# Kernel optimization log

Hardware: AMD Instinct MI355X
Metric: run time of the kernel (lower is better)

Reference implementation:

```python
import jax, jax.numpy as jnp
import numpy as np

N = 50000      # nodes
E = 800000     # edges
T = 2000000    # triplets
FE = 64        # num_edge_features
FT = 64        # num_triplet_features
CUTOFF = 6.0   # cutoff_triplet
EPS = 1e-5     # BatchNorm1d eps


def setup_inputs() -> dict:
    key = jax.random.key(0)
    ks = jax.random.split(key, 20)
    rn = lambda k, shape, s=1.0: jax.random.normal(k, shape, dtype=jnp.float32) * s
    inp = {}
    inp["pos"] = rn(ks[0], (N, 3), 3.0)
    inp["nbr_shift"] = rn(ks[1], (E, 3), 0.1)
    inp["edge_attr"] = rn(ks[2], (E, FE))
    inp["triplet_attr"] = rn(ks[3], (T, FT))
    inp["eW"] = rn(ks[4], (2, FE, FE), 0.1)
    inp["eb"] = rn(ks[5], (2, FE), 0.1)
    inp["eg"] = jnp.ones((2, FE), jnp.float32)
    inp["ebeta"] = jnp.zeros((2, FE), jnp.float32)
    inp["em"] = jnp.zeros((2, FE), jnp.float32)   # BN running mean
    inp["ev"] = jnp.ones((2, FE), jnp.float32)    # BN running var
    inp["eWo"] = rn(ks[6], (FE, 1), 0.1)
    inp["ebo"] = rn(ks[7], (1,), 0.1)
    inp["tW"] = rn(ks[8], (2, FT, FT), 0.1)
    inp["tb"] = rn(ks[9], (2, FT), 0.1)
    inp["tg"] = jnp.ones((2, FT), jnp.float32)
    inp["tbeta"] = jnp.zeros((2, FT), jnp.float32)
    inp["tm"] = jnp.zeros((2, FT), jnp.float32)
    inp["tv"] = jnp.ones((2, FT), jnp.float32)
    inp["tWo"] = rn(ks[10], (FT, 1), 0.1)
    inp["tbo"] = rn(ks[11], (1,), 0.1)
    # graph indices
    inp["edge_index"] = jax.random.randint(ks[12], (2, E), 0, N)
    inp["idx_j"] = jax.random.randint(ks[13], (T,), 0, N)    # node index
    inp["idx_kj"] = jax.random.randint(ks[14], (T,), 0, E)   # edge index
    inp["idx_ji"] = jax.random.randint(ks[15], (T,), 0, E)   # edge index
    return inp


def _mlp(x, W, b, g, bt, m, v, Wo, bo):
    for l in range(W.shape[0]):
        h = x @ W[l] + b[l]
        h = (h - m[l]) * jax.lax.rsqrt(v[l] + EPS) * g[l] + bt[l]
        x = jax.nn.softplus(h)
    return x @ Wo + bo


def reference(pos, nbr_shift, edge_attr, triplet_attr,
              eW, eb, eg, ebeta, em, ev, eWo, ebo,
              tW, tb, tg, tbeta, tm, tv, tWo, tbo,
              edge_index, idx_j, idx_kj, idx_ji):
    j_idx, i_idx = edge_index[0], edge_index[1]
    edge_dir = pos[i_idx] + nbr_shift - pos[j_idx]              # [E,3]
    edge_length = jnp.sqrt(jnp.sum(edge_dir * edge_dir, -1))    # [E]
    edge_dir = edge_dir / edge_length[:, None]
    # symmetric dyad d_ji d_ji^T, flattened to [E,9]
    dyad_ji = (edge_dir[:, :, None] * edge_dir[:, None, :]).reshape(-1, 9)
    temp_sym = _mlp(edge_attr, eW, eb, eg, ebeta, em, ev, eWo, ebo) * dyad_ji
    born = jax.ops.segment_sum(temp_sym, i_idx, num_segments=N)  # [N,9]
    # triplet cross dyad d_kj d_ji^T, masked by cutoff on both edge lengths
    d_kj = edge_dir[idx_kj]
    d_ji = edge_dir[idx_ji]
    dyad_cross = (d_kj[:, :, None] * d_ji[:, None, :]).reshape(-1, 9)  # [T,9]
    mask = ((edge_length[idx_kj] < CUTOFF) & (edge_length[idx_ji] < CUTOFF))
    mask = mask.astype(temp_sym.dtype)[:, None]
    temp_cross = _mlp(triplet_attr, tW, tb, tg, tbeta, tm, tv, tWo, tbo) * mask * dyad_cross
    born = born + jax.ops.segment_sum(temp_cross, idx_j, num_segments=N)
    return born
```

## Files before the change

### kernel.cpp

```cpp
#include <hip/hip_runtime.h>
#include <hip/hip_bf16.h>

#define NN 50000
#define NE 800000
#define NT 2000000
#define CUT 6.0f

#define ITEMS_PER_WAVE 2048
#define NWAVES ((NT + ITEMS_PER_WAVE - 1) / ITEMS_PER_WAVE)

#define EDGE_BLOCKS 1792
#define TRIP_BLOCKS 832

#define WS_EPASS  12800000
#define WS_CNT    13600000
#define WS_WCNT   13600064
#define WS_WOFF   13604160
#define WS_BMASK  13608256
#define WS_LIST   13858256

typedef __attribute__((ext_vector_type(8))) short short8;
typedef __attribute__((ext_vector_type(4))) float f32x4;

__device__ __forceinline__ short bf16_of(float f) {
    unsigned u = __float_as_uint(f);
    unsigned r = (u + 0x7fffu + ((u >> 16) & 1u)) >> 16;
    return (short)r;
}

__device__ __forceinline__ float softplus_f(float x) {
    float t = __expf(-fabsf(x));
    return fmaxf(x, 0.0f) + __logf(1.0f + t);
}

__device__ __forceinline__ short8 to_bf8(float4 u, float4 v) {
    short8 r;
    r[0] = bf16_of(u.x); r[1] = bf16_of(u.y); r[2] = bf16_of(u.z); r[3] = bf16_of(u.w);
    r[4] = bf16_of(v.x); r[5] = bf16_of(v.y); r[6] = bf16_of(v.z); r[7] = bf16_of(v.w);
    return r;
}

struct MlpW {
    short8 wb[2][2][4];
    float bias[2][4];
    float wo[4];
    float bo;
};

struct PF {
    float4 x0, x1, x2, x3;
    float4 dv;
    int tgt;
};

__device__ __forceinline__ void load_weights(
    const float* __restrict__ W, const float* __restrict__ b,
    const float* __restrict__ g, const float* __restrict__ bt,
    const float* __restrict__ m, const float* __restrict__ v,
    const float* __restrict__ Wo, const float* __restrict__ bo, MlpW& w) {
    const int lane = threadIdx.x & 63;
    const int grp = lane >> 4, c = lane & 15;
#pragma unroll
    for (int l = 0; l < 2; ++l)
#pragma unroll
        for (int nt = 0; nt < 4; ++nt) {
            int j = nt * 16 + c;
            float s = g[l * 64 + j] * rsqrtf(v[l * 64 + j] + 1e-5f);
            w.bias[l][nt] = (b[l * 64 + j] - m[l * 64 + j]) * s + bt[l * 64 + j];
#pragma unroll
            for (int kt = 0; kt < 2; ++kt) {
                short8 f;
#pragma unroll
                for (int i = 0; i < 8; ++i)
                    f[i] = bf16_of(W[l * 4096 + (kt * 32 + grp * 8 + i) * 64 + j] * s);
                w.wb[l][kt][nt] = f;
            }
        }
#pragma unroll
    for (int nt = 0; nt < 4; ++nt) w.wo[nt] = Wo[nt * 16 + c];
    w.bo = bo[0];
}

__device__ __forceinline__ void pf_edge(int tile, const float* __restrict__ edge_attr,
                                        const float4* __restrict__ dirlen,
                                        const int* __restrict__ edge_index, PF& p) {
    const int lane = threadIdx.x & 63;
    const int grp = lane >> 4, c = lane & 15;
    const float4* rp = (const float4*)(edge_attr + (size_t)(tile * 16 + c) * 64 + grp * 8);
    p.x0 = rp[0]; p.x1 = rp[1]; p.x2 = rp[8]; p.x3 = rp[9];
    if (grp <= 1) {
        p.dv = dirlen[tile * 16 + c];
    } else if (grp == 2) {
        p.tgt = edge_index[NE + tile * 16 + c];
    }
}

__device__ __forceinline__ void pf_trip(int tile, int cnt, const float* __restrict__ trip_attr,
                                        const float4* __restrict__ dirlen,
                                        const int* __restrict__ idx_j,
                                        const int* __restrict__ idx_kj,
                                        const int* __restrict__ idx_ji,
                                        const int* __restrict__ list, PF& p) {
    const int lane = threadIdx.x & 63;
    const int grp = lane >> 4, c = lane & 15;
    int g = tile * 16 + c;
    bool valid = g < cnt;
    int trow = list[valid ? g : 0];
    const float4* rp = (const float4*)(trip_attr + (size_t)trow * 64 + grp * 8);
    p.x0 = rp[0]; p.x1 = rp[1]; p.x2 = rp[8]; p.x3 = rp[9];
    if (grp == 0) {
        p.dv = dirlen[idx_kj[trow]];
    } else if (grp == 1) {
        p.dv = dirlen[idx_ji[trow]];
    } else if (grp == 2) {
        p.tgt = valid ? idx_j[trow] : -1;
    }
}

__device__ __forceinline__ void tile_compute(const PF& p, const MlpW& w,
                                             unsigned short* lds, float (*sdata)[9],
                                             float* __restrict__ out) {
    const int lane = threadIdx.x & 63;
    const int grp = lane >> 4, c = lane & 15;
    short8 a0 = to_bf8(p.x0, p.x1), a1 = to_bf8(p.x2, p.x3);
    f32x4 acc[4];
#pragma unroll
    for (int nt = 0; nt < 4; ++nt) {
        f32x4 z = {0.f, 0.f, 0.f, 0.f};
        z = __builtin_amdgcn_mfma_f32_16x16x32_bf16(a0, w.wb[0][0][nt], z, 0, 0, 0);
        z = __builtin_amdgcn_mfma_f32_16x16x32_bf16(a1, w.wb[0][1][nt], z, 0, 0, 0);
        acc[nt] = z;
    }
#pragma unroll
    for (int nt = 0; nt < 4; ++nt)
#pragma unroll
        for (int r = 0; r < 4; ++r) {
            float y = softplus_f(acc[nt][r] + w.bias[0][nt]);
            int row = grp * 4 + r;
            int byte = (row * 128 + (nt * 16 + c) * 2) ^ ((row & 7) << 4);
            *(unsigned short*)((char*)lds + byte) = (unsigned short)bf16_of(y);
        }
    asm volatile("s_waitcnt lgkmcnt(0)" ::: "memory");
    short8 b0 = *(const short8*)((char*)lds + ((c * 128 + grp * 16) ^ ((c & 7) << 4)));
    short8 b1 = *(const short8*)((char*)lds + ((c * 128 + 64 + grp * 16) ^ ((c & 7) << 4)));
    f32x4 acc2[4];
#pragma unroll
    for (int nt = 0; nt < 4; ++nt) {
        f32x4 z = {0.f, 0.f, 0.f, 0.f};
        z = __builtin_amdgcn_mfma_f32_16x16x32_bf16(b0, w.wb[1][0][nt], z, 0, 0, 0);
        z = __builtin_amdgcn_mfma_f32_16x16x32_bf16(b1, w.wb[1][1][nt], z, 0, 0, 0);
        acc2[nt] = z;
    }
    float ps[4] = {0.f, 0.f, 0.f, 0.f};
#pragma unroll
    for (int nt = 0; nt < 4; ++nt)
#pragma unroll
        for (int r = 0; r < 4; ++r) {
            float y = softplus_f(acc2[nt][r] + w.bias[1][nt]);
            ps[r] = fmaf(y, w.wo[nt], ps[r]);
        }
#pragma unroll
    for (int msk = 1; msk < 16; msk <<= 1)
#pragma unroll
        for (int r = 0; r < 4; ++r) ps[r] += __shfl_xor(ps[r], msk);
    if (c == 0) {
#pragma unroll
        for (int r = 0; r < 4; ++r) sdata[grp * 4 + r][6] = ps[r] + w.bo;
    }
    if (grp == 0) {
        sdata[c][0] = p.dv.x; sdata[c][1] = p.dv.y; sdata[c][2] = p.dv.z;
    } else if (grp == 1) {
        sdata[c][3] = p.dv.x; sdata[c][4] = p.dv.y; sdata[c][5] = p.dv.z;
    } else if (grp == 2) {
        sdata[c][7] = __int_as_float(p.tgt);
    }
    asm volatile("s_waitcnt lgkmcnt(0)" ::: "memory");
#pragma unroll
    for (int ph = 0; ph < 3; ++ph) {
        int idx = ph * 64 + lane;
        if (idx < 144) {
            int el = idx / 9;
            int comp = idx - el * 9;
            int a = comp / 3, b2 = comp - a * 3;
            const float* sd = sdata[el];
            int tgt = __float_as_int(sd[7]);
            if (tgt >= 0) {
                float val = sd[6] * sd[a] * sd[3 + b2];
                atomicAdd(&out[tgt * 9 + comp], val);
            }
        }
    }
}

__global__ void geom_kernel(const float* __restrict__ pos,
                            const float* __restrict__ nbr_shift,
                            const int* __restrict__ edge_index,
                            float4* __restrict__ dirlen,
                            unsigned char* __restrict__ epass) {
    int e = blockIdx.x * blockDim.x + threadIdx.x;
    if (e >= NE) return;
    int j = edge_index[e];
    int i = edge_index[NE + e];
    float dx = __fsub_rn(__fadd_rn(pos[i * 3 + 0], nbr_shift[e * 3 + 0]), pos[j * 3 + 0]);
    float dy = __fsub_rn(__fadd_rn(pos[i * 3 + 1], nbr_shift[e * 3 + 1]), pos[j * 3 + 1]);
    float dz = __fsub_rn(__fadd_rn(pos[i * 3 + 2], nbr_shift[e * 3 + 2]), pos[j * 3 + 2]);
    float l2 = __fadd_rn(__fadd_rn(__fmul_rn(dx, dx), __fmul_rn(dy, dy)), __fmul_rn(dz, dz));
    float len = __fsqrt_rn(l2);
    float4 o;
    o.x = __fdiv_rn(dx, len);
    o.y = __fdiv_rn(dy, len);
    o.z = __fdiv_rn(dz, len);
    o.w = len;
    dirlen[e] = o;
    epass[e] = (len < CUT) ? 1 : 0;
}

__global__ __launch_bounds__(64) void compact_count(
    const int* __restrict__ idx_kj, const int* __restrict__ idx_ji,
    const unsigned char* __restrict__ epass, int* __restrict__ waveCounts,
    unsigned long long* __restrict__ bitmask) {
    const int b = blockIdx.x;
    const int lane = threadIdx.x;
    const int base = b * ITEMS_PER_WAVE;
    int cnt = 0;
#pragma unroll 4
    for (int k = 0; k < ITEMS_PER_WAVE / 64; ++k) {
        int t = base + k * 64 + lane;
        bool pass = false;
        if (t < NT)
            pass = (epass[idx_kj[t]] & epass[idx_ji[t]]) != 0;
        unsigned long long bal = __ballot(pass);
        if (lane == 0) bitmask[b * 32 + k] = bal;
        cnt += __popcll(bal);
    }
    if (lane == 0) waveCounts[b] = cnt;
}

__global__ __launch_bounds__(1024) void scan_kernel(const int* __restrict__ waveCounts,
                                                    int* __restrict__ waveOffsets,
                                                    int* __restrict__ counter) {
    __shared__ int s[1024];
    const int t = threadIdx.x;
    int c = (t < NWAVES) ? waveCounts[t] : 0;
    s[t] = c;
    __syncthreads();
#pragma unroll
    for (int off = 1; off < 1024; off <<= 1) {
        int v = (t >= off) ? s[t - off] : 0;
        __syncthreads();
        s[t] += v;
        __syncthreads();
    }
    if (t < NWAVES) waveOffsets[t] = s[t] - c;
    if (t == NWAVES - 1) *counter = s[t];
}

__global__ __launch_bounds__(64) void compact_write(
    const unsigned long long* __restrict__ bitmask, const int* __restrict__ waveOffsets,
    int* __restrict__ list) {
    const int b = blockIdx.x;
    const int lane = threadIdx.x;
    const int base = b * ITEMS_PER_WAVE;
    int run = waveOffsets[b];
    const unsigned long long lt = (1ull << lane) - 1ull;
#pragma unroll 4
    for (int k = 0; k < ITEMS_PER_WAVE / 64; ++k) {
        unsigned long long bal = bitmask[b * 32 + k];
        if ((bal >> lane) & 1ull)
            list[run + __popcll(bal & lt)] = base + k * 64 + lane;
        run += __popcll(bal);
    }
}

__global__ __launch_bounds__(256) void mlp_kernel(
    const float* __restrict__ edge_attr, const float* __restrict__ trip_attr,
    const float* __restrict__ eW, const float* __restrict__ eb,
    const float* __restrict__ eg, const float* __restrict__ ebeta,
    const float* __restrict__ em, const float* __restrict__ ev,
    const float* __restrict__ eWo, const float* __restrict__ ebo,
    const float* __restrict__ tW, const float* __restrict__ tb,
    const float* __restrict__ tg, const float* __restrict__ tbeta,
    const float* __restrict__ tm, const float* __restrict__ tv,
    const float* __restrict__ tWo, const float* __restrict__ tbo,
    const int* __restrict__ edge_index, const int* __restrict__ idx_j,
    const int* __restrict__ idx_kj, const int* __restrict__ idx_ji,
    const float4* __restrict__ dirlen, const int* __restrict__ counter,
    const int* __restrict__ list, float* __restrict__ out) {
    __shared__ __align__(16) unsigned short lds_t[4][1024];
    __shared__ __align__(16) float sdata[4][16][9];
    const int wave = threadIdx.x >> 6;
    unsigned short* lds = &lds_t[wave][0];
    float (*sd)[9] = sdata[wave];
    MlpW w;
    PF cur, nxt;
    if (blockIdx.x < EDGE_BLOCKS) {
        load_weights(eW, eb, eg, ebeta, em, ev, eWo, ebo, w);
        const int gwave = blockIdx.x * 4 + wave;
        const int stride = EDGE_BLOCKS * 4;
        const int ntiles = NE / 16;
        int tile = gwave;
        if (tile < ntiles) pf_edge(tile, edge_attr, dirlen, edge_index, cur);
        for (; tile < ntiles; tile += stride) {
            int tn = tile + stride;
            if (tn < ntiles) pf_edge(tn, edge_attr, dirlen, edge_index, nxt);
            tile_compute(cur, w, lds, sd, out);
            cur = nxt;
        }
    } else {
        load_weights(tW, tb, tg, tbeta, tm, tv, tWo, tbo, w);
        const int cnt = *counter;
        const int gwave = (blockIdx.x - EDGE_BLOCKS) * 4 + wave;
        const int stride = TRIP_BLOCKS * 4;
        const int ntiles = (cnt + 15) / 16;
        int tile = gwave;
        if (tile < ntiles) pf_trip(tile, cnt, trip_attr, dirlen, idx_j, idx_kj, idx_ji, list, cur);
        for (; tile < ntiles; tile += stride) {
            int tn = tile + stride;
            if (tn < ntiles) pf_trip(tn, cnt, trip_attr, dirlen, idx_j, idx_kj, idx_ji, list, nxt);
            tile_compute(cur, w, lds, sd, out);
            cur = nxt;
        }
    }
}

extern "C" void kernel_launch(void* const* d_in, const int* in_sizes, int n_in,
                              void* d_out, int out_size, void* d_ws, size_t ws_size,
                              hipStream_t stream) {
    const float* pos       = (const float*)d_in[0];
    const float* nbr_shift = (const float*)d_in[1];
    const float* edge_attr = (const float*)d_in[2];
    const float* trip_attr = (const float*)d_in[3];
    const float* eW    = (const float*)d_in[4];
    const float* eb    = (const float*)d_in[5];
    const float* eg    = (const float*)d_in[6];
    const float* ebeta = (const float*)d_in[7];
    const float* em    = (const float*)d_in[8];
    const float* ev    = (const float*)d_in[9];
    const float* eWo   = (const float*)d_in[10];
    const float* ebo   = (const float*)d_in[11];
    const float* tW    = (const float*)d_in[12];
    const float* tb    = (const float*)d_in[13];
    const float* tg    = (const float*)d_in[14];
    const float* tbeta = (const float*)d_in[15];
    const float* tm    = (const float*)d_in[16];
    const float* tv    = (const float*)d_in[17];
    const float* tWo   = (const float*)d_in[18];
    const float* tbo   = (const float*)d_in[19];
    const int* edge_index = (const int*)d_in[20];
    const int* idx_j      = (const int*)d_in[21];
    const int* idx_kj     = (const int*)d_in[22];
    const int* idx_ji     = (const int*)d_in[23];
    float* out = (float*)d_out;

    char* ws = (char*)d_ws;
    float4* dirlen        = (float4*)ws;
    unsigned char* epass  = (unsigned char*)(ws + WS_EPASS);
    int* counter          = (int*)(ws + WS_CNT);
    int* waveCounts       = (int*)(ws + WS_WCNT);
    int* waveOffsets      = (int*)(ws + WS_WOFF);
    unsigned long long* bm = (unsigned long long*)(ws + WS_BMASK);
    int* list             = (int*)(ws + WS_LIST);

    hipMemsetAsync(d_out, 0, (size_t)out_size * sizeof(float), stream);
    geom_kernel<<<(NE + 255) / 256, 256, 0, stream>>>(pos, nbr_shift, edge_index, dirlen, epass);
    compact_count<<<NWAVES, 64, 0, stream>>>(idx_kj, idx_ji, epass, waveCounts, bm);
    scan_kernel<<<1, 1024, 0, stream>>>(waveCounts, waveOffsets, counter);
    compact_write<<<NWAVES, 64, 0, stream>>>(bm, waveOffsets, list);
    mlp_kernel<<<EDGE_BLOCKS + TRIP_BLOCKS, 256, 0, stream>>>(
        edge_attr, trip_attr,
        eW, eb, eg, ebeta, em, ev, eWo, ebo,
        tW, tb, tg, tbeta, tm, tv, tWo, tbo,
        edge_index, idx_j, idx_kj, idx_ji,
        dirlen, counter, list, out);
}
```

Baseline: 229.3 us.

## Process two MLP tiles per wave iteration and use hardware bf16 conversion

Each wave now handles a pair of 16-row tiles per loop iteration and interleaves their MFMA, softplus and reduction chains, so two independent dependency chains can hide each other's latency. The geometry direction vectors and target indices are no longer prefetched one iteration ahead. They are loaded just before compute, which shrinks the prefetch registers but puts the dependent gather latency (list→idx→dirlen) back on the critical path. The manual bf16 rounding is also replaced with __float2bfloat16, and LDS per block doubles.

```diff
diff --git a/kernel.cpp b/kernel.cpp
--- a/kernel.cpp
+++ b/kernel.cpp
@@ -11,6 +11,7 @@
 
 #define EDGE_BLOCKS 1792
 #define TRIP_BLOCKS 832
+#define EDGE_PAIRS (NE / 32)
 
 #define WS_EPASS  12800000
 #define WS_CNT    13600000
@@ -22,10 +23,9 @@
 typedef __attribute__((ext_vector_type(8))) short short8;
 typedef __attribute__((ext_vector_type(4))) float f32x4;
 
-__device__ __forceinline__ short bf16_of(float f) {
-    unsigned u = __float_as_uint(f);
-    unsigned r = (u + 0x7fffu + ((u >> 16) & 1u)) >> 16;
-    return (short)r;
+__device__ __forceinline__ short bf16hw(float f) {
+    __hip_bfloat16 h = __float2bfloat16(f);
+    return *reinterpret_cast<short*>(&h);
 }
 
 __device__ __forceinline__ float softplus_f(float x) {
@@ -35,8 +35,8 @@
 
 __device__ __forceinline__ short8 to_bf8(float4 u, float4 v) {
     short8 r;
-    r[0] = bf16_of(u.x); r[1] = bf16_of(u.y); r[2] = bf16_of(u.z); r[3] = bf16_of(u.w);
-    r[4] = bf16_of(v.x); r[5] = bf16_of(v.y); r[6] = bf16_of(v.z); r[7] = bf16_of(v.w);
+    r[0] = bf16hw(u.x); r[1] = bf16hw(u.y); r[2] = bf16hw(u.z); r[3] = bf16hw(u.w);
+    r[4] = bf16hw(v.x); r[5] = bf16hw(v.y); r[6] = bf16hw(v.z); r[7] = bf16hw(v.w);
     return r;
 }
 
@@ -47,11 +47,7 @@
     float bo;
 };
 
-struct PF {
-    float4 x0, x1, x2, x3;
-    float4 dv;
-    int tgt;
-};
+struct PF { float4 x0, x1, x2, x3; };
 
 __device__ __forceinline__ void load_weights(
     const float* __restrict__ W, const float* __restrict__ b,
@@ -72,7 +68,7 @@
                 short8 f;
 #pragma unroll
                 for (int i = 0; i < 8; ++i)
-                    f[i] = bf16_of(W[l * 4096 + (kt * 32 + grp * 8 + i) * 64 + j] * s);
+                    f[i] = bf16hw(W[l * 4096 + (kt * 32 + grp * 8 + i) * 64 + j] * s);
                 w.wb[l][kt][nt] = f;
             }
         }
@@ -81,112 +77,103 @@
     w.bo = bo[0];
 }
 
-__device__ __forceinline__ void pf_edge(int tile, const float* __restrict__ edge_attr,
-                                        const float4* __restrict__ dirlen,
-                                        const int* __restrict__ edge_index, PF& p) {
+__device__ __forceinline__ void pf_x(const float* __restrict__ base, size_t row, PF& p) {
+    const int lane = threadIdx.x & 63;
+    const int grp = lane >> 4;
+    const float4* rp = (const float4*)(base + row * 64 + grp * 8);
+    p.x0 = rp[0]; p.x1 = rp[1]; p.x2 = rp[8]; p.x3 = rp[9];
+}
+
+__device__ __forceinline__ void pair_core(
+    const PF& pA, const PF& pB, float4 dvA, float4 dvB, int tgtA, int tgtB,
+    const MlpW& w, unsigned short* ldsA, unsigned short* ldsB,
+    float (*sdA)[9], float (*sdB)[9], float* __restrict__ out) {
     const int lane = threadIdx.x & 63;
     const int grp = lane >> 4, c = lane & 15;
-    const float4* rp = (const float4*)(edge_attr + (size_t)(tile * 16 + c) * 64 + grp * 8);
-    p.x0 = rp[0]; p.x1 = rp[1]; p.x2 = rp[8]; p.x3 = rp[9];
-    if (grp <= 1) {
-        p.dv = dirlen[tile * 16 + c];
-    } else if (grp == 2) {
-        p.tgt = edge_index[NE + tile * 16 + c];
-    }
-}
-
-__device__ __forceinline__ void pf_trip(int tile, int cnt, const float* __restrict__ trip_attr,
-                                        const float4* __restrict__ dirlen,
-                                        const int* __restrict__ idx_j,
-                                        const int* __restrict__ idx_kj,
-                                        const int* __restrict__ idx_ji,
-                                        const int* __restrict__ list, PF& p) {
-    const int lane = threadIdx.x & 63;
-    const int grp = lane >> 4, c = lane & 15;
-    int g = tile * 16 + c;
-    bool valid = g < cnt;
-    int trow = list[valid ? g : 0];
-    const float4* rp = (const float4*)(trip_attr + (size_t)trow * 64 + grp * 8);
-    p.x0 = rp[0]; p.x1 = rp[1]; p.x2 = rp[8]; p.x3 = rp[9];
-    if (grp == 0) {
-        p.dv = dirlen[idx_kj[trow]];
-    } else if (grp == 1) {
-        p.dv = dirlen[idx_ji[trow]];
-    } else if (grp == 2) {
-        p.tgt = valid ? idx_j[trow] : -1;
-    }
-}
-
-__device__ __forceinline__ void tile_compute(const PF& p, const MlpW& w,
-                                             unsigned short* lds, float (*sdata)[9],
-                                             float* __restrict__ out) {
-    const int lane = threadIdx.x & 63;
-    const int grp = lane >> 4, c = lane & 15;
-    short8 a0 = to_bf8(p.x0, p.x1), a1 = to_bf8(p.x2, p.x3);
-    f32x4 acc[4];
+    short8 aA0 = to_bf8(pA.x0, pA.x1), aA1 = to_bf8(pA.x2, pA.x3);
+    short8 aB0 = to_bf8(pB.x0, pB.x1), aB1 = to_bf8(pB.x2, pB.x3);
+    f32x4 accA[4], accB[4];
 #pragma unroll
     for (int nt = 0; nt < 4; ++nt) {
-        f32x4 z = {0.f, 0.f, 0.f, 0.f};
-        z = __builtin_amdgcn_mfma_f32_16x16x32_bf16(a0, w.wb[0][0][nt], z, 0, 0, 0);
-        z = __builtin_amdgcn_mfma_f32_16x16x32_bf16(a1, w.wb[0][1][nt], z, 0, 0, 0);
-        acc[nt] = z;
+        f32x4 zA = {0.f, 0.f, 0.f, 0.f}, zB = {0.f, 0.f, 0.f, 0.f};
+        zA = __builtin_amdgcn_mfma_f32_16x16x32_bf16(aA0, w.wb[0][0][nt], zA, 0, 0, 0);
+        zB = __builtin_amdgcn_mfma_f32_16x16x32_bf16(aB0, w.wb[0][0][nt], zB, 0, 0, 0);
+        zA = __builtin_amdgcn_mfma_f32_16x16x32_bf16(aA1, w.wb[0][1][nt], zA, 0, 0, 0);
+        zB = __builtin_amdgcn_mfma_f32_16x16x32_bf16(aB1, w.wb[0][1][nt], zB, 0, 0, 0);
+        accA[nt] = zA; accB[nt] = zB;
     }
 #pragma unroll
     for (int nt = 0; nt < 4; ++nt)
 #pragma unroll
         for (int r = 0; r < 4; ++r) {
-            float y = softplus_f(acc[nt][r] + w.bias[0][nt]);
             int row = grp * 4 + r;
             int byte = (row * 128 + (nt * 16 + c) * 2) ^ ((row & 7) << 4);
-            *(unsigned short*)((char*)lds + byte) = (unsigned short)bf16_of(y);
+            float yA = softplus_f(accA[nt][r] + w.bias[0][nt]);
+            float yB = softplus_f(accB[nt][r] + w.bias[0][nt]);
+            *(unsigned short*)((char*)ldsA + byte) = (unsigned short)bf16hw(yA);
+            *(unsigned short*)((char*)ldsB + byte) = (unsigned short)bf16hw(yB);
         }
     asm volatile("s_waitcnt lgkmcnt(0)" ::: "memory");
-    short8 b0 = *(const short8*)((char*)lds + ((c * 128 + grp * 16) ^ ((c & 7) << 4)));
-    short8 b1 = *(const short8*)((char*)lds + ((c * 128 + 64 + grp * 16) ^ ((c & 7) << 4)));
-    f32x4 acc2[4];
+    int by0 = (c * 128 + grp * 16) ^ ((c & 7) << 4);
+    int by1 = (c * 128 + 64 + grp * 16) ^ ((c & 7) << 4);
+    short8 bA0 = *(const short8*)((char*)ldsA + by0);
+    short8 bA1 = *(const short8*)((char*)ldsA + by1);
+    short8 bB0 = *(const short8*)((char*)ldsB + by0);
+    short8 bB1 = *(const short8*)((char*)ldsB + by1);
+    f32x4 acc2A[4], acc2B[4];
 #pragma unroll
     for (int nt = 0; nt < 4; ++nt) {
-        f32x4 z = {0.f, 0.f, 0.f, 0.f};
-        z = __builtin_amdgcn_mfma_f32_16x16x32_bf16(b0, w.wb[1][0][nt], z, 0, 0, 0);
-        z = __builtin_amdgcn_mfma_f32_16x16x32_bf16(b1, w.wb[1][1][nt], z, 0, 0, 0);
-        acc2[nt] = z;
-    }
-    float ps[4] = {0.f, 0.f, 0.f, 0.f};
+        f32x4 zA = {0.f, 0.f, 0.f, 0.f}, zB = {0.f, 0.f, 0.f, 0.f};
+        zA = __builtin_amdgcn_mfma_f32_16x16x32_bf16(bA0, w.wb[1][0][nt], zA, 0, 0, 0);
+        zB = __builtin_amdgcn_mfma_f32_16x16x32_bf16(bB0, w.wb[1][0][nt], zB, 0, 0, 0);
+        zA = __builtin_amdgcn_mfma_f32_16x16x32_bf16(bA1, w.wb[1][1][nt], zA, 0, 0, 0);
+        zB = __builtin_amdgcn_mfma_f32_16x16x32_bf16(bB1, w.wb[1][1][nt], zB, 0, 0, 0);
+        acc2A[nt] = zA; acc2B[nt] = zB;
+    }
+    float psA[4] = {0.f, 0.f, 0.f, 0.f}, psB[4] = {0.f, 0.f, 0.f, 0.f};
 #pragma unroll
     for (int nt = 0; nt < 4; ++nt)
 #pragma unroll
         for (int r = 0; r < 4; ++r) {
-            float y = softplus_f(acc2[nt][r] + w.bias[1][nt]);
-            ps[r] = fmaf(y, w.wo[nt], ps[r]);
+            psA[r] = fmaf(softplus_f(acc2A[nt][r] + w.bias[1][nt]), w.wo[nt], psA[r]);
+            psB[r] = fmaf(softplus_f(acc2B[nt][r] + w.bias[1][nt]), w.wo[nt], psB[r]);
         }
 #pragma unroll
     for (int msk = 1; msk < 16; msk <<= 1)
 #pragma unroll
-        for (int r = 0; r < 4; ++r) ps[r] += __shfl_xor(ps[r], msk);
+        for (int r = 0; r < 4; ++r) {
+            psA[r] += __shfl_xor(psA[r], msk);
+            psB[r] += __shfl_xor(psB[r], msk);
+        }
     if (c == 0) {
 #pragma unroll
-        for (int r = 0; r < 4; ++r) sdata[grp * 4 + r][6] = ps[r] + w.bo;
+        for (int r = 0; r < 4; ++r) {
+            sdA[grp * 4 + r][6] = psA[r] + w.bo;
+            sdB[grp * 4 + r][6] = psB[r] + w.bo;
+        }
     }
     if (grp == 0) {
-        sdata[c][0] = p.dv.x; sdata[c][1] = p.dv.y; sdata[c][2] = p.dv.z;
+        sdA[c][0] = dvA.x; sdA[c][1] = dvA.y; sdA[c][2] = dvA.z;
+        sdB[c][0] = dvB.x; sdB[c][1] = dvB.y; sdB[c][2] = dvB.z;
     } else if (grp == 1) {
-        sdata[c][3] = p.dv.x; sdata[c][4] = p.dv.y; sdata[c][5] = p.dv.z;
+        sdA[c][3] = dvA.x; sdA[c][4] = dvA.y; sdA[c][5] = dvA.z;
+        sdB[c][3] = dvB.x; sdB[c][4] = dvB.y; sdB[c][5] = dvB.z;
     } else if (grp == 2) {
-        sdata[c][7] = __int_as_float(p.tgt);
+        sdA[c][7] = __int_as_float(tgtA);
+        sdB[c][7] = __int_as_float(tgtB);
     }
     asm volatile("s_waitcnt lgkmcnt(0)" ::: "memory");
 #pragma unroll
-    for (int ph = 0; ph < 3; ++ph) {
+    for (int ph = 0; ph < 5; ++ph) {
         int idx = ph * 64 + lane;
-        if (idx < 144) {
-            int el = idx / 9;
-            int comp = idx - el * 9;
-            int a = comp / 3, b2 = comp - a * 3;
-            const float* sd = sdata[el];
+        if (idx < 288) {
+            int el2 = idx / 9;
+            int comp = idx - el2 * 9;
+            const float* sd = (el2 < 16) ? sdA[el2] : sdB[el2 - 16];
             int tgt = __float_as_int(sd[7]);
             if (tgt >= 0) {
-                float val = sd[6] * sd[a] * sd[3 + b2];
-                atomicAdd(&out[tgt * 9 + comp], val);
+                int a = comp / 3, b2 = comp - a * 3;
+                atomicAdd(&out[tgt * 9 + comp], sd[6] * sd[a] * sd[3 + b2]);
             }
         }
     }
@@ -286,39 +273,69 @@
     const int* __restrict__ idx_kj, const int* __restrict__ idx_ji,
     const float4* __restrict__ dirlen, const int* __restrict__ counter,
     const int* __restrict__ list, float* __restrict__ out) {
-    __shared__ __align__(16) unsigned short lds_t[4][1024];
-    __shared__ __align__(16) float sdata[4][16][9];
+    __shared__ __align__(16) unsigned short lds_t[4][2][1024];
+    __shared__ __align__(16) float sdata[4][2][16][9];
     const int wave = threadIdx.x >> 6;
-    unsigned short* lds = &lds_t[wave][0];
-    float (*sd)[9] = sdata[wave];
+    const int lane = threadIdx.x & 63;
+    const int grp = lane >> 4, c = lane & 15;
+    unsigned short* ldsA = &lds_t[wave][0][0];
+    unsigned short* ldsB = &lds_t[wave][1][0];
+    float (*sdA)[9] = sdata[wave][0];
+    float (*sdB)[9] = sdata[wave][1];
     MlpW w;
-    PF cur, nxt;
+    PF cA, cB, nA, nB;
     if (blockIdx.x < EDGE_BLOCKS) {
         load_weights(eW, eb, eg, ebeta, em, ev, eWo, ebo, w);
         const int gwave = blockIdx.x * 4 + wave;
         const int stride = EDGE_BLOCKS * 4;
-        const int ntiles = NE / 16;
-        int tile = gwave;
-        if (tile < ntiles) pf_edge(tile, edge_attr, dirlen, edge_index, cur);
-        for (; tile < ntiles; tile += stride) {
-            int tn = tile + stride;
-            if (tn < ntiles) pf_edge(tn, edge_attr, dirlen, edge_index, nxt);
-            tile_compute(cur, w, lds, sd, out);
-            cur = nxt;
+        int p = gwave;
+        if (p < EDGE_PAIRS) {
+            pf_x(edge_attr, (size_t)(2 * p) * 16 + c, cA);
+            pf_x(edge_attr, (size_t)(2 * p + 1) * 16 + c, cB);
+        }
+        for (; p < EDGE_PAIRS; p += stride) {
+            int pn = p + stride;
+            if (pn < EDGE_PAIRS) {
+                pf_x(edge_attr, (size_t)(2 * pn) * 16 + c, nA);
+                pf_x(edge_attr, (size_t)(2 * pn + 1) * 16 + c, nB);
+            }
+            int eA = (2 * p) * 16 + c, eB = (2 * p + 1) * 16 + c;
+            float4 dvA = make_float4(0, 0, 0, 0), dvB = dvA;
+            int tgtA = -1, tgtB = -1;
+            if (grp <= 1) { dvA = dirlen[eA]; dvB = dirlen[eB]; }
+            else if (grp == 2) { tgtA = edge_index[NE + eA]; tgtB = edge_index[NE + eB]; }
+            pair_core(cA, cB, dvA, dvB, tgtA, tgtB, w, ldsA, ldsB, sdA, sdB, out);
+            cA = nA; cB = nB;
         }
     } else {
         load_weights(tW, tb, tg, tbeta, tm, tv, tWo, tbo, w);
         const int cnt = *counter;
+        const int npairs = (cnt + 31) / 32;
         const int gwave = (blockIdx.x - EDGE_BLOCKS) * 4 + wave;
         const int stride = TRIP_BLOCKS * 4;
-        const int ntiles = (cnt + 15) / 16;
-        int tile = gwave;
-        if (tile < ntiles) pf_trip(tile, cnt, trip_attr, dirlen, idx_j, idx_kj, idx_ji, list, cur);
-        for (; tile < ntiles; tile += stride) {
-            int tn = tile + stride;
-            if (tn < ntiles) pf_trip(tn, cnt, trip_attr, dirlen, idx_j, idx_kj, idx_ji, list, nxt);
-            tile_compute(cur, w, lds, sd, out);
-            cur = nxt;
+        int p = gwave;
+        if (p < npairs) {
+            int gA = (2 * p) * 16 + c, gB = (2 * p + 1) * 16 + c;
+            pf_x(trip_attr, (size_t)list[gA < cnt ? gA : 0], cA);
+            pf_x(trip_attr, (size_t)list[gB < cnt ? gB : 0], cB);
+        }
+        for (; p < npairs; p += stride) {
+            int pn = p + stride;
+            if (pn < npairs) {
+                int gA = (2 * pn) * 16 + c, gB = (2 * pn + 1) * 16 + c;
+                pf_x(trip_attr, (size_t)list[gA < cnt ? gA : 0], nA);
+                pf_x(trip_attr, (size_t)list[gB < cnt ? gB : 0], nB);
+            }
+            int gA = (2 * p) * 16 + c, gB = (2 * p + 1) * 16 + c;
+            bool vA = gA < cnt, vB = gB < cnt;
+            int trA = list[vA ? gA : 0], trB = list[vB ? gB : 0];
+            float4 dvA = make_float4(0, 0, 0, 0), dvB = dvA;
+            int tgtA = -1, tgtB = -1;
+            if (grp == 0) { dvA = dirlen[idx_kj[trA]]; dvB = dirlen[idx_kj[trB]]; }
+            else if (grp == 1) { dvA = dirlen[idx_ji[trA]]; dvB = dirlen[idx_ji[trB]]; }
+            else if (grp == 2) { tgtA = vA ? idx_j[trA] : -1; tgtB = vB ? idx_j[trB] : -1; }
+            pair_core(cA, cB, dvA, dvB, tgtA, tgtB, w, ldsA, ldsB, sdA, sdB, out);
+            cA = nA; cB = nB;
         }
     }
 }
@@ -353,13 +370,13 @@
     float* out = (float*)d_out;
 
     char* ws = (char*)d_ws;
-    float4* dirlen        = (float4*)ws;
-    unsigned char* epass  = (unsigned char*)(ws + WS_EPASS);
-    int* counter          = (int*)(ws + WS_CNT);
-    int* waveCounts       = (int*)(ws + WS_WCNT);
-    int* waveOffsets      = (int*)(ws + WS_WOFF);
+    float4* dirlen         = (float4*)ws;
+    unsigned char* epass   = (unsigned char*)(ws + WS_EPASS);
+    int* counter           = (int*)(ws + WS_CNT);
+    int* waveCounts        = (int*)(ws + WS_WCNT);
+    int* waveOffsets       = (int*)(ws + WS_WOFF);
     unsigned long long* bm = (unsigned long long*)(ws + WS_BMASK);
-    int* list             = (int*)(ws + WS_LIST);
+    int* list              = (int*)(ws + WS_LIST);
 
     hipMemsetAsync(d_out, 0, (size_t)out_size * sizeof(float), stream);
     geom_kernel<<<(NE + 255) / 256, 256, 0, stream>>>(pos, nbr_shift, edge_index, dirlen, epass);
```

Result: slower. 367.4 us (+60.2%).

## Split MLP and scatter into separate kernels, use hardware bf16 conversion

Applied to the files above, without the earlier changes.

The MLP kernel now writes only the per-row scalar outputs to workspace buffers. A new scatter kernel then reads the direction vectors and targets, forms the 9 dyad products and does the atomic adds, one thread per edge or triplet. This takes the gathers, the LDS staging and the atomics out of the MFMA loop. The cost is an extra kernel launch plus a global write and re-read of the scalars. The change also folds the bias into the MFMA accumulator initialisation and swaps the manual bf16 rounding for the library conversion.

```diff
diff --git a/kernel.cpp b/kernel.cpp
--- a/kernel.cpp
+++ b/kernel.cpp
@@ -18,14 +18,15 @@
 #define WS_WOFF   13604160
 #define WS_BMASK  13608256
 #define WS_LIST   13858256
+#define WS_SEDGE  21858256
+#define WS_STRIP  25058256
 
 typedef __attribute__((ext_vector_type(8))) short short8;
 typedef __attribute__((ext_vector_type(4))) float f32x4;
 
-__device__ __forceinline__ short bf16_of(float f) {
-    unsigned u = __float_as_uint(f);
-    unsigned r = (u + 0x7fffu + ((u >> 16) & 1u)) >> 16;
-    return (short)r;
+__device__ __forceinline__ unsigned short bf16hw(float f) {
+    __hip_bfloat16 h = __float2bfloat16(f);
+    return *reinterpret_cast<unsigned short*>(&h);
 }
 
 __device__ __forceinline__ float softplus_f(float x) {
@@ -35,8 +36,8 @@
 
 __device__ __forceinline__ short8 to_bf8(float4 u, float4 v) {
     short8 r;
-    r[0] = bf16_of(u.x); r[1] = bf16_of(u.y); r[2] = bf16_of(u.z); r[3] = bf16_of(u.w);
-    r[4] = bf16_of(v.x); r[5] = bf16_of(v.y); r[6] = bf16_of(v.z); r[7] = bf16_of(v.w);
+    r[0] = bf16hw(u.x); r[1] = bf16hw(u.y); r[2] = bf16hw(u.z); r[3] = bf16hw(u.w);
+    r[4] = bf16hw(v.x); r[5] = bf16hw(v.y); r[6] = bf16hw(v.z); r[7] = bf16hw(v.w);
     return r;
 }
 
@@ -47,11 +48,7 @@
     float bo;
 };
 
-struct PF {
-    float4 x0, x1, x2, x3;
-    float4 dv;
-    int tgt;
-};
+struct PF { float4 x0, x1, x2, x3; };
 
 __device__ __forceinline__ void load_weights(
     const float* __restrict__ W, const float* __restrict__ b,
@@ -72,7 +69,7 @@
                 short8 f;
 #pragma unroll
                 for (int i = 0; i < 8; ++i)
-                    f[i] = bf16_of(W[l * 4096 + (kt * 32 + grp * 8 + i) * 64 + j] * s);
+                    f[i] = (short)bf16hw(W[l * 4096 + (kt * 32 + grp * 8 + i) * 64 + j] * s);
                 w.wb[l][kt][nt] = f;
             }
         }
@@ -81,52 +78,22 @@
     w.bo = bo[0];
 }
 
-__device__ __forceinline__ void pf_edge(int tile, const float* __restrict__ edge_attr,
-                                        const float4* __restrict__ dirlen,
-                                        const int* __restrict__ edge_index, PF& p) {
-    const int lane = threadIdx.x & 63;
-    const int grp = lane >> 4, c = lane & 15;
-    const float4* rp = (const float4*)(edge_attr + (size_t)(tile * 16 + c) * 64 + grp * 8);
+__device__ __forceinline__ void pf_x(const float* __restrict__ base, size_t row, PF& p) {
+    const int grp = (threadIdx.x & 63) >> 4;
+    const float4* rp = (const float4*)(base + row * 64 + grp * 8);
     p.x0 = rp[0]; p.x1 = rp[1]; p.x2 = rp[8]; p.x3 = rp[9];
-    if (grp <= 1) {
-        p.dv = dirlen[tile * 16 + c];
-    } else if (grp == 2) {
-        p.tgt = edge_index[NE + tile * 16 + c];
-    }
-}
-
-__device__ __forceinline__ void pf_trip(int tile, int cnt, const float* __restrict__ trip_attr,
-                                        const float4* __restrict__ dirlen,
-                                        const int* __restrict__ idx_j,
-                                        const int* __restrict__ idx_kj,
-                                        const int* __restrict__ idx_ji,
-                                        const int* __restrict__ list, PF& p) {
-    const int lane = threadIdx.x & 63;
-    const int grp = lane >> 4, c = lane & 15;
-    int g = tile * 16 + c;
-    bool valid = g < cnt;
-    int trow = list[valid ? g : 0];
-    const float4* rp = (const float4*)(trip_attr + (size_t)trow * 64 + grp * 8);
-    p.x0 = rp[0]; p.x1 = rp[1]; p.x2 = rp[8]; p.x3 = rp[9];
-    if (grp == 0) {
-        p.dv = dirlen[idx_kj[trow]];
-    } else if (grp == 1) {
-        p.dv = dirlen[idx_ji[trow]];
-    } else if (grp == 2) {
-        p.tgt = valid ? idx_j[trow] : -1;
-    }
-}
-
-__device__ __forceinline__ void tile_compute(const PF& p, const MlpW& w,
-                                             unsigned short* lds, float (*sdata)[9],
-                                             float* __restrict__ out) {
+}
+
+__device__ __forceinline__ void mlp_tile(const PF& p, const MlpW& w,
+                                         unsigned short* lds, float ps[4]) {
     const int lane = threadIdx.x & 63;
     const int grp = lane >> 4, c = lane & 15;
     short8 a0 = to_bf8(p.x0, p.x1), a1 = to_bf8(p.x2, p.x3);
     f32x4 acc[4];
 #pragma unroll
     for (int nt = 0; nt < 4; ++nt) {
-        f32x4 z = {0.f, 0.f, 0.f, 0.f};
+        float b = w.bias[0][nt];
+        f32x4 z = {b, b, b, b};
         z = __builtin_amdgcn_mfma_f32_16x16x32_bf16(a0, w.wb[0][0][nt], z, 0, 0, 0);
         z = __builtin_amdgcn_mfma_f32_16x16x32_bf16(a1, w.wb[0][1][nt], z, 0, 0, 0);
         acc[nt] = z;
@@ -135,10 +102,10 @@
     for (int nt = 0; nt < 4; ++nt)
 #pragma unroll
         for (int r = 0; r < 4; ++r) {
-            float y = softplus_f(acc[nt][r] + w.bias[0][nt]);
+            float y = softplus_f(acc[nt][r]);
             int row = grp * 4 + r;
             int byte = (row * 128 + (nt * 16 + c) * 2) ^ ((row & 7) << 4);
-            *(unsigned short*)((char*)lds + byte) = (unsigned short)bf16_of(y);
+            *(unsigned short*)((char*)lds + byte) = bf16hw(y);
         }
     asm volatile("s_waitcnt lgkmcnt(0)" ::: "memory");
     short8 b0 = *(const short8*)((char*)lds + ((c * 128 + grp * 16) ^ ((c & 7) << 4)));
@@ -146,50 +113,25 @@
     f32x4 acc2[4];
 #pragma unroll
     for (int nt = 0; nt < 4; ++nt) {
-        f32x4 z = {0.f, 0.f, 0.f, 0.f};
+        float b = w.bias[1][nt];
+        f32x4 z = {b, b, b, b};
         z = __builtin_amdgcn_mfma_f32_16x16x32_bf16(b0, w.wb[1][0][nt], z, 0, 0, 0);
         z = __builtin_amdgcn_mfma_f32_16x16x32_bf16(b1, w.wb[1][1][nt], z, 0, 0, 0);
         acc2[nt] = z;
     }
-    float ps[4] = {0.f, 0.f, 0.f, 0.f};
+#pragma unroll
+    for (int r = 0; r < 4; ++r) ps[r] = 0.f;
 #pragma unroll
     for (int nt = 0; nt < 4; ++nt)
 #pragma unroll
-        for (int r = 0; r < 4; ++r) {
-            float y = softplus_f(acc2[nt][r] + w.bias[1][nt]);
-            ps[r] = fmaf(y, w.wo[nt], ps[r]);
-        }
+        for (int r = 0; r < 4; ++r)
+            ps[r] = fmaf(softplus_f(acc2[nt][r]), w.wo[nt], ps[r]);
 #pragma unroll
     for (int msk = 1; msk < 16; msk <<= 1)
 #pragma unroll
         for (int r = 0; r < 4; ++r) ps[r] += __shfl_xor(ps[r], msk);
-    if (c == 0) {
-#pragma unroll
-        for (int r = 0; r < 4; ++r) sdata[grp * 4 + r][6] = ps[r] + w.bo;
-    }
-    if (grp == 0) {
-        sdata[c][0] = p.dv.x; sdata[c][1] = p.dv.y; sdata[c][2] = p.dv.z;
-    } else if (grp == 1) {
-        sdata[c][3] = p.dv.x; sdata[c][4] = p.dv.y; sdata[c][5] = p.dv.z;
-    } else if (grp == 2) {
-        sdata[c][7] = __int_as_float(p.tgt);
-    }
-    asm volatile("s_waitcnt lgkmcnt(0)" ::: "memory");
-#pragma unroll
-    for (int ph = 0; ph < 3; ++ph) {
-        int idx = ph * 64 + lane;
-        if (idx < 144) {
-            int el = idx / 9;
-            int comp = idx - el * 9;
-            int a = comp / 3, b2 = comp - a * 3;
-            const float* sd = sdata[el];
-            int tgt = __float_as_int(sd[7]);
-            if (tgt >= 0) {
-                float val = sd[6] * sd[a] * sd[3 + b2];
-                atomicAdd(&out[tgt * 9 + comp], val);
-            }
-        }
-    }
+#pragma unroll
+    for (int r = 0; r < 4; ++r) ps[r] += w.bo;
 }
 
 __global__ void geom_kernel(const float* __restrict__ pos,
@@ -282,28 +224,31 @@
     const float* __restrict__ tg, const float* __restrict__ tbeta,
     const float* __restrict__ tm, const float* __restrict__ tv,
     const float* __restrict__ tWo, const float* __restrict__ tbo,
-    const int* __restrict__ edge_index, const int* __restrict__ idx_j,
-    const int* __restrict__ idx_kj, const int* __restrict__ idx_ji,
-    const float4* __restrict__ dirlen, const int* __restrict__ counter,
-    const int* __restrict__ list, float* __restrict__ out) {
+    const int* __restrict__ counter, const int* __restrict__ list,
+    float* __restrict__ s_edge, float* __restrict__ s_trip) {
     __shared__ __align__(16) unsigned short lds_t[4][1024];
-    __shared__ __align__(16) float sdata[4][16][9];
     const int wave = threadIdx.x >> 6;
+    const int lane = threadIdx.x & 63;
+    const int grp = lane >> 4, c = lane & 15;
     unsigned short* lds = &lds_t[wave][0];
-    float (*sd)[9] = sdata[wave];
     MlpW w;
     PF cur, nxt;
+    float ps[4];
     if (blockIdx.x < EDGE_BLOCKS) {
         load_weights(eW, eb, eg, ebeta, em, ev, eWo, ebo, w);
         const int gwave = blockIdx.x * 4 + wave;
         const int stride = EDGE_BLOCKS * 4;
         const int ntiles = NE / 16;
         int tile = gwave;
-        if (tile < ntiles) pf_edge(tile, edge_attr, dirlen, edge_index, cur);
+        if (tile < ntiles) pf_x(edge_attr, (size_t)tile * 16 + c, cur);
         for (; tile < ntiles; tile += stride) {
             int tn = tile + stride;
-            if (tn < ntiles) pf_edge(tn, edge_attr, dirlen, edge_index, nxt);
-            tile_compute(cur, w, lds, sd, out);
+            if (tn < ntiles) pf_x(edge_attr, (size_t)tn * 16 + c, nxt);
+            mlp_tile(cur, w, lds, ps);
+            if (c == 0) {
+#pragma unroll
+                for (int r = 0; r < 4; ++r) s_edge[tile * 16 + grp * 4 + r] = ps[r];
+            }
             cur = nxt;
         }
     } else {
@@ -313,13 +258,63 @@
         const int stride = TRIP_BLOCKS * 4;
         const int ntiles = (cnt + 15) / 16;
         int tile = gwave;
-        if (tile < ntiles) pf_trip(tile, cnt, trip_attr, dirlen, idx_j, idx_kj, idx_ji, list, cur);
+        if (tile < ntiles) {
+            int g = tile * 16 + c;
+            pf_x(trip_attr, (size_t)list[g < cnt ? g : 0], cur);
+        }
         for (; tile < ntiles; tile += stride) {
             int tn = tile + stride;
-            if (tn < ntiles) pf_trip(tn, cnt, trip_attr, dirlen, idx_j, idx_kj, idx_ji, list, nxt);
-            tile_compute(cur, w, lds, sd, out);
+            if (tn < ntiles) {
+                int g = tn * 16 + c;
+                pf_x(trip_attr, (size_t)list[g < cnt ? g : 0], nxt);
+            }
+            mlp_tile(cur, w, lds, ps);
+            if (c == 0) {
+#pragma unroll
+                for (int r = 0; r < 4; ++r) {
+                    int g = tile * 16 + grp * 4 + r;
+                    if (g < cnt) s_trip[g] = ps[r];
+                }
+            }
             cur = nxt;
         }
+    }
+}
+
+__global__ __launch_bounds__(256) void scatter_kernel(
+    const float* __restrict__ s_edge, const float* __restrict__ s_trip,
+    const float4* __restrict__ dirlen, const int* __restrict__ edge_index,
+    const int* __restrict__ idx_j, const int* __restrict__ idx_kj,
+    const int* __restrict__ idx_ji, const int* __restrict__ counter,
+    const int* __restrict__ list, float* __restrict__ out) {
+    const int cnt = *counter;
+    const int total = NE + cnt;
+    const int stride = gridDim.x * blockDim.x;
+    for (int i = blockIdx.x * blockDim.x + threadIdx.x; i < total; i += stride) {
+        float s;
+        float4 dk, dj;
+        int tgt;
+        if (i < NE) {
+            s = s_edge[i];
+            dk = dirlen[i];
+            dj = dk;
+            tgt = edge_index[NE + i];
+        } else {
+            int ii = i - NE;
+            int t = list[ii];
+            s = s_trip[ii];
+            dk = dirlen[idx_kj[t]];
+            dj = dirlen[idx_ji[t]];
+            tgt = idx_j[t];
+        }
+        float dka[3] = {dk.x, dk.y, dk.z};
+        float dja[3] = {dj.x, dj.y, dj.z};
+        float* op = out + (size_t)tgt * 9;
+#pragma unroll
+        for (int a = 0; a < 3; ++a)
+#pragma unroll
+            for (int b2 = 0; b2 < 3; ++b2)
+                atomicAdd(&op[a * 3 + b2], s * dka[a] * dja[b2]);
     }
 }
 
@@ -353,13 +348,15 @@
     float* out = (float*)d_out;
 
     char* ws = (char*)d_ws;
-    float4* dirlen        = (float4*)ws;
-    unsigned char* epass  = (unsigned char*)(ws + WS_EPASS);
-    int* counter          = (int*)(ws + WS_CNT);
-    int* waveCounts       = (int*)(ws + WS_WCNT);
-    int* waveOffsets      = (int*)(ws + WS_WOFF);
+    float4* dirlen         = (float4*)ws;
+    unsigned char* epass   = (unsigned char*)(ws + WS_EPASS);
+    int* counter           = (int*)(ws + WS_CNT);
+    int* waveCounts        = (int*)(ws + WS_WCNT);
+    int* waveOffsets       = (int*)(ws + WS_WOFF);
     unsigned long long* bm = (unsigned long long*)(ws + WS_BMASK);
-    int* list             = (int*)(ws + WS_LIST);
+    int* list              = (int*)(ws + WS_LIST);
+    float* s_edge          = (float*)(ws + WS_SEDGE);
+    float* s_trip          = (float*)(ws + WS_STRIP);
 
     hipMemsetAsync(d_out, 0, (size_t)out_size * sizeof(float), stream);
     geom_kernel<<<(NE + 255) / 256, 256, 0, stream>>>(pos, nbr_shift, edge_index, dirlen, epass);
@@ -370,6 +367,7 @@
         edge_attr, trip_attr,
         eW, eb, eg, ebeta, em, ev, eWo, ebo,
         tW, tb, tg, tbeta, tm, tv, tWo, tbo,
-        edge_index, idx_j, idx_kj, idx_ji,
-        dirlen, counter, list, out);
-}
+        counter, list, s_edge, s_trip);
+    scatter_kernel<<<2048, 256, 0, stream>>>(s_edge, s_trip, dirlen, edge_index,
+                                             idx_j, idx_kj, idx_ji, counter, list, out);
+}
```

New measurement: 724.7 us. +216.1%, slower.
